# Kernel tuning notes

Measured on AMD Instinct MI355X. Metric: run time of the kernel, lower is better.

Reference implementation:

```python
import jax, jax.numpy as jnp
import numpy as np

N = 20000      # num_sr == num_tg entities
D = 256        # ent_dim
DR = 256       # rel_dim
RNUM = 1000    # number of relations
Q = 128        # SVD rank
H = 4          # n_head
L = 2          # layers
E_RAND = 640000  # random edges (avg degree 32); N self-loops appended
LEAK = 0.2
EPS_LN = 1e-5


def _l2norm(x):
    # F.normalize(x, dim=1, p=2)
    return x / jnp.maximum(jnp.linalg.norm(x, axis=1, keepdims=True), 1e-12)


def _gat(x, src, dst, W, a_s, a_d):
    """Multi-head GAT layer on an edge list; heads are averaged so out dim == in dim.
    x: [N,D], W: [H,D,D], a_s/a_d: [H,D]."""
    n = x.shape[0]
    h = jnp.einsum('nd,hde->nhe', x, W)                  # [N,H,D]
    es = jnp.einsum('nhe,he->nh', h, a_s)                # [N,H]
    ed = jnp.einsum('nhe,he->nh', h, a_d)                # [N,H]
    e = jax.nn.leaky_relu(es[src] + ed[dst], LEAK)       # [E,H]
    # segment softmax over incoming edges of each dst node
    m = jax.ops.segment_max(e, dst, num_segments=n)      # [N,H]
    ex = jnp.exp(e - m[dst])
    den = jax.ops.segment_sum(ex, dst, num_segments=n)   # [N,H]
    attn = ex / (den[dst] + 1e-16)                       # [E,H]
    out = jax.ops.segment_sum(attn[:, :, None] * h[src], dst, num_segments=n)  # [N,H,D]
    return jax.nn.elu(out).mean(axis=1)                  # head average -> [N,D]


def _mha(x, wq, bq, wk, bk, wv, bv, fc_w, fc_b, ln_g, ln_b):
    """Standard post-norm multi-head self-attention over the 'ranges' axis. x: [N,R,D]."""
    n, r, d = x.shape
    def split(y):  # [N,R,H*D] -> [N,H,R,D]
        return y.reshape(n, r, H, d).transpose(0, 2, 1, 3)
    q, k, v = split(x @ wq + bq), split(x @ wk + bk), split(x @ wv + bv)
    attn = jax.nn.softmax(jnp.einsum('nhqd,nhkd->nhqk', q, k) / jnp.sqrt(jnp.float32(d)), axis=-1)
    o = jnp.einsum('nhqk,nhkd->nhqd', attn, v).transpose(0, 2, 1, 3).reshape(n, r, H * d)
    o = o @ fc_w + fc_b + x                              # output proj + residual
    mu = o.mean(-1, keepdims=True)
    var = o.var(-1, keepdims=True)
    return (o - mu) / jnp.sqrt(var + EPS_LN) * ln_g + ln_b


def _rel_agg(adj_in, adj_out, rel):
    # sparse-dense mm + row-sum normalize + concat (direct=True branch)
    ri = (adj_in @ rel) / (adj_in.sum(-1, keepdims=True) + 1e-5)
    ro = (adj_out @ rel) / (adj_out.sum(-1, keepdims=True) + 1e-5)
    return jnp.concatenate([ri, ro], axis=-1)            # [N, 2*DR]


def _forward(ent_sr, ent_tg, rel_sr, rel_tg, alpha,
             u_mul_s_sr, vt_sr, u_mul_s_tg, vt_tg,
             rel_adj_sr_in, rel_adj_sr_out, rel_adj_tg_in, rel_adj_tg_out,
             gat_W, gat_a_src, gat_a_dst,
             wq, bq, wk, bk, wv, bv, fc_w, fc_b, ln_g, ln_b,
             edges_sr, edges_tg):
    # --- Relation Aggregator (direct=True, phase='eval': aug == aggregated) ---
    sr_rel = _rel_agg(rel_adj_sr_in, rel_adj_sr_out, rel_sr)
    tg_rel = _rel_agg(rel_adj_tg_in, rel_adj_tg_out, rel_tg)
    aug_sr_rel, aug_tg_rel = sr_rel, tg_rel

    # --- Global Structure Aggregator: SVD-based propagation ---
    e_sr, e_tg = ent_sr, ent_tg
    for _ in range(L):
        g_sr = u_mul_s_sr @ (vt_sr @ e_sr)               # [N,Q]@([Q,N]@[N,D])
        g_tg = u_mul_s_tg @ (vt_tg @ e_tg)
        e_sr = jax.nn.relu(alpha * g_sr + (1.0 - alpha) * e_sr)
        e_tg = jax.nn.relu(alpha * g_tg + (1.0 - alpha) * e_tg)
    aug_sr = e_sr + ent_sr
    aug_tg = e_tg + ent_tg

    # --- Attentive Neighbor Aggregator (res=True; eval => dropout = identity) ---
    x_sr, x_tg = ent_sr, ent_tg
    sr_list, tg_list = [x_sr], [x_tg]
    for l in range(L):
        x_sr = _l2norm(_gat(x_sr, edges_sr[0], edges_sr[1], gat_W[l], gat_a_src[l], gat_a_dst[l]))
        x_tg = _l2norm(_gat(x_tg, edges_tg[0], edges_tg[1], gat_W[l], gat_a_src[l], gat_a_dst[l]))
        sr_list.append(x_sr)
        tg_list.append(x_tg)

    # --- multi-range neighborhood fusion ---
    sr = _mha(jnp.stack(sr_list, axis=1), wq, bq, wk, bk, wv, bv, fc_w, fc_b, ln_g, ln_b).mean(axis=1)
    tg = _mha(jnp.stack(tg_list, axis=1), wq, bq, wk, bk, wv, bv, fc_w, fc_b, ln_g, ln_b).mean(axis=1)

    # --- final fusion: neighbors + relation semantics ---
    sr_out = jnp.concatenate([sr, sr_rel], axis=-1)
    tg_out = jnp.concatenate([tg, tg_rel], axis=-1)
    aug_sr_out = jnp.concatenate([aug_sr, aug_sr_rel], axis=-1)
    aug_tg_out = jnp.concatenate([aug_tg, aug_tg_rel], axis=-1)
    return (sr_out, tg_out, aug_sr_out, aug_tg_out)


def setup_inputs() -> dict:
    key = jax.random.key(0)
    ks = jax.random.split(key, 32)
    def nrm(k, shape, s):
        return jax.random.normal(k, shape, jnp.float32) * s
    def edges(k):
        e = jax.random.randint(k, (2, E_RAND), 0, N, dtype=jnp.int32)
        loops = jnp.arange(N, dtype=jnp.int32)
        return jnp.concatenate([e, jnp.stack([loops, loops])], axis=1)  # [2, E_RAND+N]
    inp = {
        'ent_sr': nrm(ks[0], (N, D), 0.1),
        'ent_tg': nrm(ks[1], (N, D), 0.1),
        'rel_sr': nrm(ks[2], (RNUM, DR), 0.1),
        'rel_tg': nrm(ks[3], (RNUM, DR), 0.1),
        'alpha': jnp.float32(0.5),
        'u_mul_s_sr': nrm(ks[4], (N, Q), 0.05),
        'vt_sr': nrm(ks[5], (Q, N), 0.05),
        'u_mul_s_tg': nrm(ks[6], (N, Q), 0.05),
        'vt_tg': nrm(ks[7], (Q, N), 0.05),
        'rel_adj_sr_in': jax.random.uniform(ks[8], (N, RNUM), jnp.float32),
        'rel_adj_sr_out': jax.random.uniform(ks[9], (N, RNUM), jnp.float32),
        'rel_adj_tg_in': jax.random.uniform(ks[10], (N, RNUM), jnp.float32),
        'rel_adj_tg_out': jax.random.uniform(ks[11], (N, RNUM), jnp.float32),
        'gat_W': nrm(ks[12], (L, H, D, D), 1.0 / np.sqrt(D)),
        'gat_a_src': nrm(ks[13], (L, H, D), 1.0 / np.sqrt(D)),
        'gat_a_dst': nrm(ks[14], (L, H, D), 1.0 / np.sqrt(D)),
        'wq': nrm(ks[15], (D, H * D), 1.0 / np.sqrt(D)),
        'bq': jnp.zeros((H * D,), jnp.float32),
        'wk': nrm(ks[16], (D, H * D), 1.0 / np.sqrt(D)),
        'bk': jnp.zeros((H * D,), jnp.float32),
        'wv': nrm(ks[17], (D, H * D), 1.0 / np.sqrt(D)),
        'bv': jnp.zeros((H * D,), jnp.float32),
        'fc_w': nrm(ks[18], (H * D, D), 1.0 / np.sqrt(H * D)),
        'fc_b': jnp.zeros((D,), jnp.float32),
        'ln_g': jnp.ones((D,), jnp.float32),
        'ln_b': jnp.zeros((D,), jnp.float32),
        'edges_sr': edges(ks[19]),
        'edges_tg': edges(ks[20]),
    }
    return inp


def reference(ent_sr, ent_tg, rel_sr, rel_tg, alpha,
              u_mul_s_sr, vt_sr, u_mul_s_tg, vt_tg,
              rel_adj_sr_in, rel_adj_sr_out, rel_adj_tg_in, rel_adj_tg_out,
              gat_W, gat_a_src, gat_a_dst,
              wq, bq, wk, bk, wv, bv, fc_w, fc_b, ln_g, ln_b,
              edges_sr, edges_tg):
    return _forward(ent_sr, ent_tg, rel_sr, rel_tg, alpha,
                    u_mul_s_sr, vt_sr, u_mul_s_tg, vt_tg,
                    rel_adj_sr_in, rel_adj_sr_out, rel_adj_tg_in, rel_adj_tg_out,
                    gat_W, gat_a_src, gat_a_dst,
                    wq, bq, wk, bk, wv, bv, fc_w, fc_b, ln_g, ln_b,
                    edges_sr, edges_tg)
```

## Files before the change

### kernel.cpp

```cpp
#include <hip/hip_runtime.h>
#include <stdint.h>

typedef unsigned short u16;
typedef __bf16 bf16x8 __attribute__((ext_vector_type(8)));
typedef float f32x4 __attribute__((ext_vector_type(4)));

#define DEV static __device__ __forceinline__

DEV float bf2f(u16 u) { unsigned v = ((unsigned)u) << 16; float f; __builtin_memcpy(&f, &v, 4); return f; }
DEV u16 f2bf(float f) {
  unsigned x; __builtin_memcpy(&x, &f, 4);
  x += 0x7FFFu + ((x >> 16) & 1u);
  return (u16)(x >> 16);
}
DEV float wred_sum(float v) { for (int m = 32; m; m >>= 1) v += __shfl_xor(v, m); return v; }
DEV float wred_max(float v) { for (int m = 32; m; m >>= 1) v = fmaxf(v, __shfl_xor(v, m)); return v; }
DEV void wred_max4(f32x4& v) {
  for (int m = 32; m; m >>= 1) {
#pragma unroll
    for (int i = 0; i < 4; ++i) v[i] = fmaxf(v[i], __shfl_xor(v[i], m));
  }
}
DEV void wred_sum4(f32x4& v) {
  for (int m = 32; m; m >>= 1) {
#pragma unroll
    for (int i = 0; i < 4; ++i) v[i] += __shfl_xor(v[i], m);
  }
}

enum { M_ATOMIC = 0, M_SCALE2, M_BLEND, M_BF16, M_BF16B, M_F32B };

template <int MODE>
__global__ __launch_bounds__(256) void k_gemm(
    const u16* __restrict__ A, const u16* __restrict__ B,
    int M, int lda, int ldb, int Ksteps, int kper,
    void* __restrict__ C1v, float* __restrict__ C2, int ldc,
    const float* __restrict__ rowsum, const float* __restrict__ ein, int ldein,
    const float* __restrict__ alphap, const float* __restrict__ bias,
    long hA, long hB, long hC)
{
  __shared__ u16 As[4096], Bs[4096];
  const int tid = threadIdx.x, lane = tid & 63, wid = tid >> 6;
  const long m0 = (long)blockIdx.x * 128, n0 = (long)blockIdx.y * 128;
  int ks, kend;
  long chead = 0;
  if (hA | hB | hC) {
    A += (long)blockIdx.z * hA;
    B += (long)blockIdx.z * hB;
    chead = (long)blockIdx.z * hC;
    ks = 0; kend = Ksteps;
  } else {
    ks = blockIdx.z * kper;
    kend = ks + kper; if (kend > Ksteps) kend = Ksteps;
  }

  const u16 *ag[2], *bg[2];
  u16 *al[2], *bl[2];
#pragma unroll
  for (int i = 0; i < 2; ++i) {
    int s = (wid * 2 + i) * 64 + lane;
    int row = s >> 2, cs = (s & 3) ^ ((row >> 1) & 3);
    ag[i] = A + (m0 + row) * (long)lda + cs * 8;
    bg[i] = B + (n0 + row) * (long)ldb + cs * 8;
    al[i] = As + (wid * 2 + i) * 512;
    bl[i] = Bs + (wid * 2 + i) * 512;
  }
  const int kq = lane >> 4, rr = lane & 15;
  const int wm = wid >> 1, wn = wid & 1;

// ... 23 lines not shown
      for (int j = 0; j < 4; ++j)
        acc[i][j] = __builtin_amdgcn_mfma_f32_16x16x32_bf16(af[i], bff[j], acc[i][j], 0, 0, 0);
    __syncthreads();
  }

  float* Cf = (float*)C1v;
  u16* Cu = (u16*)C1v;
  const int r4 = (lane >> 4) << 2;
#pragma unroll
  for (int i = 0; i < 4; ++i) {
#pragma unroll
    for (int rg = 0; rg < 4; ++rg) {
      long row = m0 + wm * 64 + i * 16 + r4 + rg;
      if (row >= M) continue;
      float scale = 0.f, al_ = 0.f, ml_ = 0.f;
      if (MODE == M_SCALE2) scale = 1.f / (rowsum[row] + 1e-5f);
      if (MODE == M_BLEND) { al_ = *alphap; ml_ = 1.f - al_; }
#pragma unroll
      for (int j = 0; j < 4; ++j) {
        long col = n0 + wn * 64 + j * 16 + rr;
        float v = acc[i][j][rg];
        long idx = chead + row * (long)ldc + col;
        if (MODE == M_ATOMIC) atomicAdd(Cf + idx, v);
        else if (MODE == M_SCALE2) { float sv = v * scale; Cf[idx] = sv; C2[idx] = sv; }
        else if (MODE == M_BLEND) { float e = ein[row * (long)ldein + col]; Cf[idx] = fmaxf(al_ * v + ml_ * e, 0.f); }
        else if (MODE == M_BF16) Cu[idx] = f2bf(v);
        else if (MODE == M_BF16B) Cu[idx] = f2bf(v + bias[col]);
        else if (MODE == M_F32B) Cf[idx] = v + bias[col];
      }
    }
  }
}

__global__ void k_cvt(const float* __restrict__ in, u16* __restrict__ out, long R, long C, long Cp, long ostride)
{
  long idx = (long)blockIdx.x * blockDim.x + threadIdx.x;
  long cw = Cp >> 3;
  if (idx >= R * cw) return;
// ... 34 lines not shown
    tile[tr + i * 16][tc4 + 3] = v[3];
  }
  __syncthreads();
  int wc = t >> 4, wr4 = (t & 15) << 2;
#pragma unroll
  for (int i = 0; i < 4; ++i) {
    int c = wc + i * 16;
    u16 o[4];
#pragma unroll
    for (int k2 = 0; k2 < 4; ++k2) o[k2] = f2bf(tile[wr4 + k2][c]);
    unsigned long long pk; __builtin_memcpy(&pk, o, 8);
    *(unsigned long long*)(out + ((long)b * C + (ct << 6) + c) * Rp + (rt << 6) + wr4) = pk;
  }
}

__global__ __launch_bounds__(256) void k_adj(const float* __restrict__ in, u16* __restrict__ out,
                                             float* __restrict__ rowsum, int C, int Cp)
{
  int r = blockIdx.x, t = threadIdx.x;
  f32x4 v = {0.f, 0.f, 0.f, 0.f};
  int c = t << 2;
  if (c + 3 < C) v = *(const f32x4*)(in + (long)r * C + c);
  u16 o[4];
#pragma unroll
  for (int i = 0; i < 4; ++i) o[i] = f2bf(v[i]);
  unsigned long long pk; __builtin_memcpy(&pk, o, 8);
  *(unsigned long long*)(out + (long)r * Cp + c) = pk;
  float s = wred_sum(v[0] + v[1] + v[2] + v[3]);
  __shared__ float ws4[4];
  if ((t & 63) == 0) ws4[t >> 6] = s;
  __syncthreads();
  if (t == 0) rowsum[r] = ws4[0] + ws4[1] + ws4[2] + ws4[3];
}

__global__ void k_zero_i(int* p, int n) { for (int i = blockIdx.x * blockDim.x + threadIdx.x; i < n; i += gridDim.x * blockDim.x) p[i] = 0; }
__global__ void k_zero_f(float* p, int n) { for (int i = blockIdx.x * blockDim.x + threadIdx.x; i < n; i += gridDim.x * blockDim.x) p[i] = 0.f; }
__global__ void k_copy_i(const int* __restrict__ a, int* __restrict__ b, int n) { for (int i = blockIdx.x * blockDim.x + threadIdx.x; i < n; i += gridDim.x * blockDim.x) b[i] = a[i]; }
__global__ void k_hist(const int* __restrict__ dst, int* __restrict__ deg, int E)
{ for (int i = blockIdx.x * blockDim.x + threadIdx.x; i < E; i += gridDim.x * blockDim.x) atomicAdd(&deg[dst[i]], 1); }
__global__ void k_scatter(const int* __restrict__ src, const int* __restrict__ dst, int* __restrict__ cur,
                          int* __restrict__ srcs, int E)
{
  for (int i = blockIdx.x * blockDim.x + threadIdx.x; i < E; i += gridDim.x * blockDim.x) {
    int p = atomicAdd(&cur[dst[i]], 1);
    srcs[p] = src[i];
  }
}
__global__ void k_scan(const int* __restrict__ deg, int* __restrict__ off, int n)
{
  __shared__ int buf[1024];
  __shared__ int carry;
  int t = threadIdx.x;
  if (t == 0) { carry = 0; off[0] = 0; }
  __syncthreads();
  for (int base = 0; base < n; base += 1024) {
    int v = (base + t < n) ? deg[base + t] : 0;
    buf[t] = v;
    __syncthreads();
    for (int s = 1; s < 1024; s <<= 1) {
      int x = (t >= s) ? buf[t - s] : 0;
      __syncthreads();
      buf[t] += x;
      __syncthreads();
    }
    if (base + t < n) off[base + t + 1] = buf[t] + carry;
    int tot = buf[1023];
    __syncthreads();
    if (t == 0) carry += tot;
    __syncthreads();
  }
}

__global__ __launch_bounds__(256) void k_esed(const u16* __restrict__ h, const float* __restrict__ as_,
                                              const float* __restrict__ ad_, float* __restrict__ esq,
                                              float* __restrict__ ed, signed char* __restrict__ q8, int N)
{
  int n = blockIdx.x, t = threadIdx.x, hd = t >> 6, l = t & 63;
  long base = (long)n * 1024 + hd * 256 + (l << 2);
  ushort4 hv = *(const ushort4*)(h + base);
  float h0 = bf2f(hv.x), h1 = bf2f(hv.y), h2 = bf2f(hv.z), h3 = bf2f(hv.w);
  const float* ap = as_ + hd * 256 + (l << 2);
  const float* dp = ad_ + hd * 256 + (l << 2);
  float ps = h0 * ap[0] + h1 * ap[1] + h2 * ap[2] + h3 * ap[3];
  float pd = h0 * dp[0] + h1 * dp[1] + h2 * dp[2] + h3 * dp[3];
  ps = wred_sum(ps); pd = wred_sum(pd);
// ... 4 lines not shown
  qb[0] = (signed char)__float2int_rn(h0 * rsc);
  qb[1] = (signed char)__float2int_rn(h1 * rsc);
  qb[2] = (signed char)__float2int_rn(h2 * rsc);
  qb[3] = (signed char)__float2int_rn(h3 * rsc);
  int qw; __builtin_memcpy(&qw, qb, 4);
  *(int*)(q8 + base) = qw;
  if (l == 0) {
    esq[n * 8 + hd] = ps;
    esq[n * 8 + 4 + hd] = amax * (1.f / 127.f);
    ed[n * 4 + hd] = pd;
  }
}

__global__ __launch_bounds__(256) void k_gat(const signed char* __restrict__ q8,
                                             const float* __restrict__ esq, const float* __restrict__ ed,
                                             const int* __restrict__ off, const int* __restrict__ srcs,
                                             u16* __restrict__ xout, int N)
{
  int t = threadIdx.x, w = t >> 6, l = t & 63;
  int n = blockIdx.x * 4 + w;
  if (n >= N) return;
  int e0 = off[n], deg = off[n + 1] - e0;
  f32x4 edv = *(const f32x4*)(ed + (long)n * 4);

  f32x4 m = {-1e30f, -1e30f, -1e30f, -1e30f};
  f32x4 psum = {0.f, 0.f, 0.f, 0.f};
  f32x4 acc0 = {0.f, 0.f, 0.f, 0.f};
  f32x4 acc1 = {0.f, 0.f, 0.f, 0.f};
  f32x4 acc2 = {0.f, 0.f, 0.f, 0.f};
  f32x4 acc3 = {0.f, 0.f, 0.f, 0.f};
  const long loff = l << 2;

  for (int base = 0; base < deg; base += 64) {
    int cnt = min(64, deg - base);
    bool act = l < cnt;
    int s = 0;
    f32x4 v = {-1e30f, -1e30f, -1e30f, -1e30f};
    if (act) {
// ... 80 lines not shown
  for (int j = 0; j < 256; ++j) {
    a1 += wk[(long)d * 1024 + h * 256 + j] * bq[h * 256 + j];
    a2 += wq[(long)d * 1024 + h * 256 + j] * bk[h * 256 + j];
    a3 += bv[h * 256 + j] * fcw[(long)(h * 256 + j) * 256 + d];
  }
  vq1[t] = a1; vq2[t] = a2; beff2[t] = a3;
  if (d == 0) {
    float s = 0.f;
    for (int j = 0; j < 256; ++j) s += bq[h * 256 + j] * bk[h * 256 + j];
    s3[h] = s;
  }
}

__global__ __launch_bounds__(256) void k_score2(const u16* __restrict__ x, const u16* __restrict__ kg,
                                                const float* __restrict__ vq1, const float* __restrict__ vq2,
                                                const float* __restrict__ s3, float* __restrict__ attn, int N)
{
  int n = blockIdx.x, t = threadIdx.x, hd = t >> 6, l = t & 63;
  int i4 = l << 2;
  f32x4 xr[3], kc[3];
#pragma unroll
  for (int r = 0; r < 3; ++r) {
    ushort4 a = *(const ushort4*)(x + ((long)n * 3 + r) * 256 + i4);
    xr[r][0] = bf2f(a.x); xr[r][1] = bf2f(a.y); xr[r][2] = bf2f(a.z); xr[r][3] = bf2f(a.w);
    ushort4 b = *(const ushort4*)(kg + ((long)n * 3 + r) * 1024 + hd * 256 + i4);
    kc[r][0] = bf2f(b.x); kc[r][1] = bf2f(b.y); kc[r][2] = bf2f(b.z); kc[r][3] = bf2f(b.w);
  }
  f32x4 v1 = *(const f32x4*)(vq1 + hd * 256 + i4);
  f32x4 v2 = *(const f32x4*)(vq2 + hd * 256 + i4);
  float red[15];
#pragma unroll
  for (int r = 0; r < 3; ++r)
#pragma unroll
    for (int c = 0; c < 3; ++c) {
      f32x4 p = xr[r] * kc[c];
      red[r * 3 + c] = p[0] + p[1] + p[2] + p[3];
    }
#pragma unroll
  for (int c = 0; c < 3; ++c) {
    f32x4 p1 = xr[c] * v1;
    f32x4 p2 = xr[c] * v2;
    red[9 + c] = p1[0] + p1[1] + p1[2] + p1[3];
    red[12 + c] = p2[0] + p2[1] + p2[2] + p2[3];
  }
#pragma unroll
  for (int i = 0; i < 15; ++i) red[i] = wred_sum(red[i]);
  if (l == 0) {
    float s3h = s3[hd];
    float* out = attn + (long)n * 36 + hd * 9;
#pragma unroll
    for (int r = 0; r < 3; ++r) {
      float v0 = (red[r * 3 + 0] + red[9 + 0] + red[12 + r] + s3h) * 0.0625f;
      float v1_ = (red[r * 3 + 1] + red[9 + 1] + red[12 + r] + s3h) * 0.0625f;
      float v2_ = (red[r * 3 + 2] + red[9 + 2] + red[12 + r] + s3h) * 0.0625f;
      float mm = fmaxf(v0, fmaxf(v1_, v2_));
      float e0 = __expf(v0 - mm), e1 = __expf(v1_ - mm), e2 = __expf(v2_ - mm);
      float rs = 1.f / (e0 + e1 + e2);
      out[r * 3 + 0] = e0 * rs; out[r * 3 + 1] = e1 * rs; out[r * 3 + 2] = e2 * rs;
    }
  }
}

__global__ __launch_bounds__(256) void k_cln(const u16* __restrict__ vf, const float* __restrict__ attn,
                                             const u16* __restrict__ x, const float* __restrict__ fcb,
                                             const float* __restrict__ g, const float* __restrict__ b,
                                             float* __restrict__ out, int N)
{
  int n = blockIdx.x, t = threadIdx.x, w = t >> 6, l = t & 63;
  __shared__ float aa[36];
  __shared__ float ybuf[3][256];
  if (t < 36) aa[t] = attn[(long)n * 36 + t];
  __syncthreads();
  if (w < 3) {
    int d4 = l << 2;
    f32x4 acc = {0.f, 0.f, 0.f, 0.f};
#pragma unroll
    for (int h = 0; h < 4; ++h)
#pragma unroll
      for (int rp = 0; rp < 3; ++rp) {
        float wgt = aa[h * 9 + w * 3 + rp];
        ushort4 vv = *(const ushort4*)(vf + ((long)n * 3 + rp) * 1024 + h * 256 + d4);
        acc[0] += wgt * bf2f(vv.x); acc[1] += wgt * bf2f(vv.y);
        acc[2] += wgt * bf2f(vv.z); acc[3] += wgt * bf2f(vv.w);
      }
    f32x4 fb = *(const f32x4*)(fcb + d4);
    ushort4 xu = *(const ushort4*)(x + ((long)n * 3 + w) * 256 + d4);
    acc[0] += fb[0] + bf2f(xu.x); acc[1] += fb[1] + bf2f(xu.y);
    acc[2] += fb[2] + bf2f(xu.z); acc[3] += fb[3] + bf2f(xu.w);
    float s1 = acc[0] + acc[1] + acc[2] + acc[3];
    float s2 = acc[0] * acc[0] + acc[1] * acc[1] + acc[2] * acc[2] + acc[3] * acc[3];
    s1 = wred_sum(s1); s2 = wred_sum(s2);
    float mu = s1 * 0.00390625f;
    float var = s2 * 0.00390625f - mu * mu;
    float rs = rsqrtf(var + 1e-5f);
#pragma unroll
    for (int i = 0; i < 4; ++i) {
      int d = d4 + i;
      ybuf[w][d] = (acc[i] - mu) * rs * g[d] + b[d];
    }
  }
  __syncthreads();
  if (t < 64) {
#pragma unroll
    for (int i = 0; i < 4; ++i) {
      int d = (t << 2) + i;
      out[(long)n * 768 + d] = (ybuf[0][d] + ybuf[1][d] + ybuf[2][d]) * (1.f / 3.f);
    }
  }
}

__global__ void k_aug(const float* __restrict__ e, const float* __restrict__ ent, float* __restrict__ out, int N)
{
  long i = (long)blockIdx.x * blockDim.x + threadIdx.x;
  if (i >= (long)N * 64) return;
  long n = i >> 6; int d4 = (int)(i & 63) << 2;
  f32x4 a = *(const f32x4*)(e + n * 256 + d4);
  f32x4 c = *(const f32x4*)(ent + n * 256 + d4);
  *(f32x4*)(out + n * 768 + d4) = a + c;
}

extern "C" void kernel_launch(void* const* d_in, const int* in_sizes, int n_in,
                              void* d_out, int out_size, void* d_ws, size_t ws_size,
                              hipStream_t stream)
{
  (void)n_in; (void)out_size; (void)ws_size;
  const int N = 20000, NP = 20096, RNUM = 1000, RP = 1024;
  const int NT2 = NP + N;
  const int Es = in_sizes[26] / 2, Et = in_sizes[27] / 2;

  const float* ent_sr = (const float*)d_in[0];
  const float* ent_tg = (const float*)d_in[1];
  const float* rel_in[2] = {(const float*)d_in[2], (const float*)d_in[3]};
  const float* alphap = (const float*)d_in[4];
  const float* ums[2] = {(const float*)d_in[5], (const float*)d_in[7]};
  const float* vt[2]  = {(const float*)d_in[6], (const float*)d_in[8]};
  const float* adj[4] = {(const float*)d_in[9], (const float*)d_in[10], (const float*)d_in[11], (const float*)d_in[12]};
  const float* gat_W  = (const float*)d_in[13];
  const float* gat_as = (const float*)d_in[14];
  const float* gat_ad = (const float*)d_in[15];
  const float* wq = (const float*)d_in[16]; const float* bq = (const float*)d_in[17];
  const float* wk = (const float*)d_in[18]; const float* bk = (const float*)d_in[19];
  const float* wv = (const float*)d_in[20]; const float* bv = (const float*)d_in[21];
  const float* fcw = (const float*)d_in[22]; const float* fcb = (const float*)d_in[23];
  const float* lng = (const float*)d_in[24]; const float* lnb = (const float*)d_in[25];
  const int* edges[2] = {(const int*)d_in[26], (const int*)d_in[27]};
  const int Ecnt[2] = {Es, Et};

  float* out0 = (float*)d_out;
  float* out1 = out0 + (size_t)N * 768;
  float* out2 = out1 + (size_t)N * 768;
  float* out3 = out2 + (size_t)N * 768;

  char* wsp = (char*)d_ws; size_t wo = 0;
  auto alloc = [&](size_t bytes) { void* p = wsp + wo; wo = (wo + bytes + 255) & ~(size_t)255; return p; };

  u16* A_sr = (u16*)alloc((size_t)NP * 768 * 2);
  u16* A_tg = (u16*)alloc((size_t)NP * 768 * 2);
  u16* QBUF = (u16*)alloc((size_t)60160 * 1024 * 2);
  u16* KBUF = (u16*)alloc((size_t)60160 * 1024 * 2);
  float* OFIN = (float*)alloc((size_t)60160 * 256 * 4);
  float* rowsum = (float*)alloc((size_t)N * 4);
  u16* relT[2] = {(u16*)alloc(256 * RP * 2), (u16*)alloc(256 * RP * 2)};
  u16* WtG = (u16*)alloc((size_t)2 * 1024 * 256 * 2);
  u16* fcT = (u16*)alloc(256 * 1024 * 2);
  u16* wqB = (u16*)alloc(256 * 1024 * 2);
  u16* wkB = (u16*)alloc(256 * 1024 * 2);
  u16* wvB = (u16*)alloc(256 * 1024 * 2);
  u16* gT  = (u16*)alloc((size_t)4 * 256 * 256 * 2);
  u16* vfT = (u16*)alloc((size_t)4 * 256 * 256 * 2);
  float* vq1 = (float*)alloc(1024 * 4);
  float* vq2 = (float*)alloc(1024 * 4);
  float* beff2 = (float*)alloc(1024 * 4);
  float* s3b = (float*)alloc(4 * 4);
  float* esqb = (float*)alloc((size_t)NT2 * 8 * 4);
  float* edb = (float*)alloc((size_t)NT2 * 4 * 4);
  float* attn = (float*)alloc((size_t)N * 36 * 4);
  int* off_[2]; int* cur_[2]; int* srcs_[2];
  for (int s = 0; s < 2; ++s) {
    off_[s] = (int*)alloc((size_t)(N + 4) * 4);
    cur_[s] = (int*)alloc((size_t)(N + 4) * 4);
    srcs_[s] = (int*)alloc((size_t)Ecnt[s] * 4);
  }
  float* tT = (float*)alloc(256 * 128 * 4);
  u16* tTb = (u16*)alloc(256 * 128 * 2);

  u16* hbuf = QBUF;
  u16* adjb = (u16*)OFIN;
  float* e_b[2];
  e_b[0] = (float*)KBUF;
  e_b[1] = e_b[0] + (size_t)N * 256;
  u16* eT = (u16*)(e_b[1] + (size_t)N * 256);
  u16* vtb[2]; u16* umb[2];
  vtb[0] = eT + (size_t)256 * NP;
  vtb[1] = vtb[0] + (size_t)128 * NP;
  umb[0] = vtb[1] + (size_t)128 * NP;
  umb[1] = umb[0] + (size_t)NP * 128;
  signed char* q8buf = (signed char*)KBUF;
  u16* kgbuf = KBUF;

  u16* A_s[2] = {A_sr, A_tg};
  const float* ent_s[2] = {ent_sr, ent_tg};
  float* outm[2] = {out0, out1};
  float* outa[2] = {out2, out3};

  auto cvt = [&](const float* in, u16* out, long R, long C, long Cp, long ostr) {
    long total = R * (Cp >> 3);
    int blocks = (int)((total + 255) / 256);
    k_cvt<<<blocks, 256, 0, stream>>>(in, out, R, C, Cp, ostr);
  };
  auto cvtT = [&](const float* in, u16* out, int Bh, int R, int C, int Rp) {
    int blocks = (Rp >> 6) * (C >> 6) * Bh;
    k_cvtT<<<blocks, 256, 0, stream>>>(in, out, Bh, R, C, Rp);
  };
  auto gemm = [&](int mode, const u16* A, const u16* B, int M, int lda, int ldb, int Kp, int Nt, int splits,
                  void* C1, float* C2, int ldc, const float* rs, const float* ein, int ldein,
                  const float* alp, const float* bias, long hA = 0, long hB = 0, long hC = 0) {
    int Ks = Kp >> 5;
    int kper = (splits > 1 && !hC) ? (Ks + splits - 1) / splits : Ks;
    dim3 g((M + 127) >> 7, Nt, splits);
    switch (mode) {
      case M_ATOMIC: k_gemm<M_ATOMIC><<<g, 256, 0, stream>>>(A, B, M, lda, ldb, Ks, kper, C1, C2, ldc, rs, ein, ldein, alp, bias, hA, hB, hC); break;
      case M_SCALE2: k_gemm<M_SCALE2><<<g, 256, 0, stream>>>(A, B, M, lda, ldb, Ks, kper, C1, C2, ldc, rs, ein, ldein, alp, bias, hA, hB, hC); break;
      case M_BLEND:  k_gemm<M_BLEND><<<g, 256, 0, stream>>>(A, B, M, lda, ldb, Ks, kper, C1, C2, ldc, rs, ein, ldein, alp, bias, hA, hB, hC); break;
      case M_BF16:   k_gemm<M_BF16><<<g, 256, 0, stream>>>(A, B, M, lda, ldb, Ks, kper, C1, C2, ldc, rs, ein, ldein, alp, bias, hA, hB, hC); break;
      case M_BF16B:  k_gemm<M_BF16B><<<g, 256, 0, stream>>>(A, B, M, lda, ldb, Ks, kper, C1, C2, ldc, rs, ein, ldein, alp, bias, hA, hB, hC); break;
      case M_F32B:   k_gemm<M_F32B><<<g, 256, 0, stream>>>(A, B, M, lda, ldb, Ks, kper, C1, C2, ldc, rs, ein, ldein, alp, bias, hA, hB, hC); break;
    }
  };

  for (int s = 0; s < 2; ++s) {
    k_zero_i<<<80, 256, 0, stream>>>(cur_[s], N);
    k_hist<<<1024, 256, 0, stream>>>(edges[s] + Ecnt[s], cur_[s], Ecnt[s]);
    k_scan<<<1, 1024, 0, stream>>>(cur_[s], off_[s], N);
    k_copy_i<<<80, 256, 0, stream>>>(off_[s], cur_[s], N);
    k_scatter<<<1024, 256, 0, stream>>>(edges[s], edges[s] + Ecnt[s], cur_[s], srcs_[s], Ecnt[s]);
  }

  cvtT(rel_in[0], relT[0], 1, RNUM, 256, RP);
  cvtT(rel_in[1], relT[1], 1, RNUM, 256, RP);
  struct RelOp { const float* a; u16* rt; float* c1; float* c2; } relops[4] = {
      {adj[0], relT[0], out0 + 256, out2 + 256},
      {adj[1], relT[0], out0 + 512, out2 + 512},
      {adj[2], relT[1], out1 + 256, out3 + 256},
      {adj[3], relT[1], out1 + 512, out3 + 512},
  };
  for (int i = 0; i < 4; ++i) {
    k_adj<<<N, 256, 0, stream>>>(relops[i].a, adjb, rowsum, RNUM, RP);
    gemm(M_SCALE2, adjb, relops[i].rt, N, RP, RP, RP, 2, 1,
         relops[i].c1, relops[i].c2, 768, rowsum, nullptr, 0, nullptr, nullptr);
  }

  cvt(vt[0], vtb[0], 128, N, NP, NP);
  cvt(vt[1], vtb[1], 128, N, NP, NP);
  cvt(ums[0], umb[0], N, 128, 128, 128);
  cvt(ums[1], umb[1], N, 128, 128, 128);
  for (int s = 0; s < 2; ++s) {
    for (int l = 0; l < 2; ++l) {
      const float* esrc = l ? (const float*)e_b[s] : ent_s[s];
      cvtT(esrc, eT, 1, N, 256, NP);
      k_zero_f<<<128, 256, 0, stream>>>(tT, 256 * 128);
      gemm(M_ATOMIC, eT, vtb[s], 256, NP, NP, NP, 1, 128, tT, nullptr, 128,
           nullptr, nullptr, 0, nullptr, nullptr);
      cvt(tT, tTb, 256, 128, 128, 128);
      gemm(M_BLEND, umb[s], tTb, N, 128, 128, 128, 2, 1, e_b[s], nullptr, 256,
           nullptr, esrc, 256, alphap, nullptr);
    }
    k_aug<<<(N * 64 + 255) / 256, 256, 0, stream>>>(e_b[s], ent_s[s], outa[s], N);
  }

  cvt(ent_sr, A_sr, N, 256, 256, 768);
  cvt(ent_tg, A_tg, N, 256, 256, 768);
  cvtT(gat_W, WtG, 4, 256, 256, 256);
  cvtT(gat_W + 4 * 256 * 256, WtG + (size_t)1024 * 256, 4, 256, 256, 256);
  for (int l = 0; l < 2; ++l) {
    gemm(M_BF16, A_sr + l * 256, WtG + (size_t)l * 1024 * 256, NT2, 768, 256, 256, 8, 1,
         hbuf, nullptr, 1024, nullptr, nullptr, 0, nullptr, nullptr);
    k_esed<<<NT2, 256, 0, stream>>>(hbuf, gat_as + l * 1024, gat_ad + l * 1024, esqb, edb, q8buf, NT2);
    for (int s = 0; s < 2; ++s) {
      size_t ofs = s ? (size_t)NP : 0;
      k_gat<<<(N + 3) / 4, 256, 0, stream>>>(q8buf + ofs * 1024, esqb + ofs * 8, edb + ofs * 4,
                                             off_[s], srcs_[s], A_s[s] + (l + 1) * 256, N);
    }
  }

  cvt(wq, wqB, 256, 1024, 1024, 1024);
  cvt(wk, wkB, 256, 1024, 1024, 1024);
  cvt(wv, wvB, 256, 1024, 1024, 1024);
  cvtT(fcw, fcT, 1, 1024, 256, 1024);
  k_bias2<<<4, 256, 0, stream>>>(wq, wk, fcw, bq, bk, bv, vq1, vq2, beff2, s3b);
  gemm(M_BF16, wqB, wkB, 256, 1024, 1024, 256, 2, 4, gT, nullptr, 256,
       nullptr, nullptr, 0, nullptr, nullptr, 256, 256, 65536);
  gemm(M_BF16, fcT, wvB, 256, 1024, 1024, 256, 2, 4, vfT, nullptr, 256,
       nullptr, nullptr, 0, nullptr, nullptr, 256, 256, 65536);

  for (int s = 0; s < 2; ++s) {
    gemm(M_BF16, A_s[s], gT, 3 * N, 256, 256, 256, 8, 1, kgbuf, nullptr, 1024,
         nullptr, nullptr, 0, nullptr, nullptr);
    k_score2<<<N, 256, 0, stream>>>(A_s[s], kgbuf, vq1, vq2, s3b, attn, N);
    gemm(M_BF16B, A_s[s], vfT, 3 * N, 256, 256, 256, 8, 1, QBUF, nullptr, 1024,
         nullptr, nullptr, 0, nullptr, beff2);
    k_cln<<<N, 256, 0, stream>>>(QBUF, attn, A_s[s], fcb, lng, lnb, outm[s], N);
  }
}
```

Measured before the change: 1.926 ms.

## Batch sr/tg pipelines into merged launches and replace atomic split-K with partial reduction

Merges the separate source and target passes into single launches: k_adj4 over four adjacency matrices, batched GEMMs through a head/split z index, k_gat, k_score2, k_cln and k_aug each handle both sides via blockIdx.y. The atomic split-K GEMM for the SVD projection becomes a partial-sum GEMM (M_PART) followed by a k_red reduction kernel, which removes the zero-fill and the atomics. The prefix scan now gives each thread a serial chunk before one block scan, cutting the number of barrier rounds. This lowers launch count and the cost of small serial kernels, but uses more workspace and adds a reduction pass.

After: 1.732 ms. 1.11x faster.

```diff
diff --git a/kernel.cpp b/kernel.cpp
--- a/kernel.cpp
+++ b/kernel.cpp
@@ -28,7 +28,7 @@
   }
 }
 
-enum { M_ATOMIC = 0, M_SCALE2, M_BLEND, M_BF16, M_BF16B, M_F32B };
+enum { M_ATOMIC = 0, M_SCALE2, M_BLEND, M_BF16, M_BF16B, M_F32B, M_PART };
 
 template <int MODE>
 __global__ __launch_bounds__(256) void k_gemm(
@@ -37,22 +37,28 @@
     void* __restrict__ C1v, float* __restrict__ C2, int ldc,
     const float* __restrict__ rowsum, const float* __restrict__ ein, int ldein,
     const float* __restrict__ alphap, const float* __restrict__ bias,
-    long hA, long hB, long hC)
+    long hA, long hB, long hC, int nsplit, long hE)
 {
   __shared__ u16 As[4096], Bs[4096];
   const int tid = threadIdx.x, lane = tid & 63, wid = tid >> 6;
   const long m0 = (long)blockIdx.x * 128, n0 = (long)blockIdx.y * 128;
   int ks, kend;
   long chead = 0;
+  int hz = 0;
   if (hA | hB | hC) {
-    A += (long)blockIdx.z * hA;
-    B += (long)blockIdx.z * hB;
-    chead = (long)blockIdx.z * hC;
-    ks = 0; kend = Ksteps;
+    int z = blockIdx.z;
+    hz = z / nsplit;
+    int sp = z - hz * nsplit;
+    A += (long)hz * hA;
+    B += (long)hz * hB;
+    chead = (MODE == M_PART) ? (long)z * hC : (long)hz * hC;
+    ks = sp * kper;
+    kend = ks + kper; if (kend > Ksteps) kend = Ksteps;
   } else {
     ks = blockIdx.z * kper;
     kend = ks + kper; if (kend > Ksteps) kend = Ksteps;
   }
+  if (MODE == M_BLEND) ein += (long)hz * hE;
 
   const u16 *ag[2], *bg[2];
   u16 *al[2], *bl[2];
@@ -106,7 +112,7 @@
       long row = m0 + wm * 64 + i * 16 + r4 + rg;
       if (row >= M) continue;
       float scale = 0.f, al_ = 0.f, ml_ = 0.f;
-      if (MODE == M_SCALE2) scale = 1.f / (rowsum[row] + 1e-5f);
+      if (MODE == M_SCALE2) scale = 1.f / (rowsum[(long)hz * M + row] + 1e-5f);
       if (MODE == M_BLEND) { al_ = *alphap; ml_ = 1.f - al_; }
 #pragma unroll
       for (int j = 0; j < 4; ++j) {
@@ -114,6 +120,7 @@
         float v = acc[i][j][rg];
         long idx = chead + row * (long)ldc + col;
         if (MODE == M_ATOMIC) atomicAdd(Cf + idx, v);
+        else if (MODE == M_PART) Cf[idx] = v;
         else if (MODE == M_SCALE2) { float sv = v * scale; Cf[idx] = sv; C2[idx] = sv; }
         else if (MODE == M_BLEND) { float e = ein[row * (long)ldein + col]; Cf[idx] = fmaxf(al_ * v + ml_ * e, 0.f); }
         else if (MODE == M_BF16) Cu[idx] = f2bf(v);
@@ -178,10 +185,14 @@
   }
 }
 
-__global__ __launch_bounds__(256) void k_adj(const float* __restrict__ in, u16* __restrict__ out,
-                                             float* __restrict__ rowsum, int C, int Cp)
-{
-  int r = blockIdx.x, t = threadIdx.x;
+__global__ __launch_bounds__(256) void k_adj4(const float* __restrict__ a0, const float* __restrict__ a1,
+                                              const float* __restrict__ a2, const float* __restrict__ a3,
+                                              u16* __restrict__ o01, u16* __restrict__ o23,
+                                              float* __restrict__ rowsum, int C, int Cp, int N)
+{
+  int r = blockIdx.x, pl = blockIdx.y, t = threadIdx.x;
+  const float* in = pl == 0 ? a0 : pl == 1 ? a1 : pl == 2 ? a2 : a3;
+  u16* out = pl < 2 ? o01 + (size_t)pl * N * Cp : o23 + (size_t)(pl - 2) * N * Cp;
   f32x4 v = {0.f, 0.f, 0.f, 0.f};
   int c = t << 2;
   if (c + 3 < C) v = *(const f32x4*)(in + (long)r * C + c);
@@ -194,11 +205,20 @@
   __shared__ float ws4[4];
   if ((t & 63) == 0) ws4[t >> 6] = s;
   __syncthreads();
-  if (t == 0) rowsum[r] = ws4[0] + ws4[1] + ws4[2] + ws4[3];
+  if (t == 0) rowsum[(long)pl * N + r] = ws4[0] + ws4[1] + ws4[2] + ws4[3];
+}
+
+__global__ void k_red(const float* __restrict__ P, float* __restrict__ o, int NS)
+{
+  int i = blockIdx.x * 256 + threadIdx.x;
+  int h = i >> 15, rem = i & 32767;
+  const float* p = P + (long)h * NS * 32768 + rem;
+  float s = 0.f;
+  for (int k = 0; k < NS; ++k) s += p[(long)k * 32768];
+  o[i] = s;
 }
 
 __global__ void k_zero_i(int* p, int n) { for (int i = blockIdx.x * blockDim.x + threadIdx.x; i < n; i += gridDim.x * blockDim.x) p[i] = 0; }
-__global__ void k_zero_f(float* p, int n) { for (int i = blockIdx.x * blockDim.x + threadIdx.x; i < n; i += gridDim.x * blockDim.x) p[i] = 0.f; }
 __global__ void k_copy_i(const int* __restrict__ a, int* __restrict__ b, int n) { for (int i = blockIdx.x * blockDim.x + threadIdx.x; i < n; i += gridDim.x * blockDim.x) b[i] = a[i]; }
 __global__ void k_hist(const int* __restrict__ dst, int* __restrict__ deg, int E)
 { for (int i = blockIdx.x * blockDim.x + threadIdx.x; i < E; i += gridDim.x * blockDim.x) atomicAdd(&deg[dst[i]], 1); }
@@ -210,29 +230,25 @@
     srcs[p] = src[i];
   }
 }
-__global__ void k_scan(const int* __restrict__ deg, int* __restrict__ off, int n)
-{
-  __shared__ int buf[1024];
-  __shared__ int carry;
+__global__ __launch_bounds__(1024) void k_scan(const int* __restrict__ deg, int* __restrict__ off, int n)
+{
+  __shared__ int bsum[1024];
   int t = threadIdx.x;
-  if (t == 0) { carry = 0; off[0] = 0; }
+  int per = (n + 1023) >> 10;
+  int s0 = t * per, s1 = s0 + per; if (s1 > n) s1 = n;
+  int s = 0;
+  for (int i = s0; i < s1; ++i) s += deg[i];
+  bsum[t] = s;
   __syncthreads();
-  for (int base = 0; base < n; base += 1024) {
-    int v = (base + t < n) ? deg[base + t] : 0;
-    buf[t] = v;
+  for (int d = 1; d < 1024; d <<= 1) {
+    int x = (t >= d) ? bsum[t - d] : 0;
     __syncthreads();
-    for (int s = 1; s < 1024; s <<= 1) {
-      int x = (t >= s) ? buf[t - s] : 0;
-      __syncthreads();
-      buf[t] += x;
-      __syncthreads();
-    }
-    if (base + t < n) off[base + t + 1] = buf[t] + carry;
-    int tot = buf[1023];
+    bsum[t] += x;
     __syncthreads();
-    if (t == 0) carry += tot;
-    __syncthreads();
-  }
+  }
+  if (t == 0) off[0] = 0;
+  int run = t ? bsum[t - 1] : 0;
+  for (int i = s0; i < s1; ++i) { run += deg[i]; off[i + 1] = run; }
 }
 
 __global__ __launch_bounds__(256) void k_esed(const u16* __restrict__ h, const float* __restrict__ as_,
@@ -267,14 +283,22 @@
 
 __global__ __launch_bounds__(256) void k_gat(const signed char* __restrict__ q8,
                                              const float* __restrict__ esq, const float* __restrict__ ed,
-                                             const int* __restrict__ off, const int* __restrict__ srcs,
-                                             u16* __restrict__ xout, int N)
+                                             const int* __restrict__ off0, const int* __restrict__ srcs0,
+                                             const int* __restrict__ off1, const int* __restrict__ srcs1,
+                                             u16* __restrict__ x0, u16* __restrict__ x1, int N, int NPq)
 {
   int t = threadIdx.x, w = t >> 6, l = t & 63;
   int n = blockIdx.x * 4 + w;
   if (n >= N) return;
+  int side = blockIdx.y;
+  const int* off = side ? off1 : off0;
+  const int* srcs = side ? srcs1 : srcs0;
+  u16* xout = side ? x1 : x0;
+  size_t ofs = side ? (size_t)NPq : 0;
+  q8 += ofs * 1024; esq += ofs * 8;
+
   int e0 = off[n], deg = off[n + 1] - e0;
-  f32x4 edv = *(const f32x4*)(ed + (long)n * 4);
+  f32x4 edv = *(const f32x4*)(ed + (ofs + n) * 4);
 
   f32x4 m = {-1e30f, -1e30f, -1e30f, -1e30f};
   f32x4 psum = {0.f, 0.f, 0.f, 0.f};
@@ -385,16 +409,18 @@
 
 __global__ __launch_bounds__(256) void k_score2(const u16* __restrict__ x, const u16* __restrict__ kg,
                                                 const float* __restrict__ vq1, const float* __restrict__ vq2,
-                                                const float* __restrict__ s3, float* __restrict__ attn, int N)
-{
-  int n = blockIdx.x, t = threadIdx.x, hd = t >> 6, l = t & 63;
+                                                const float* __restrict__ s3, float* __restrict__ attn,
+                                                int N, int NPq)
+{
+  int n = blockIdx.x, side = blockIdx.y, t = threadIdx.x, hd = t >> 6, l = t & 63;
+  long rbase = (long)side * 3 * NPq + (long)n * 3;
   int i4 = l << 2;
   f32x4 xr[3], kc[3];
 #pragma unroll
   for (int r = 0; r < 3; ++r) {
-    ushort4 a = *(const ushort4*)(x + ((long)n * 3 + r) * 256 + i4);
+    ushort4 a = *(const ushort4*)(x + (rbase + r) * 256 + i4);
     xr[r][0] = bf2f(a.x); xr[r][1] = bf2f(a.y); xr[r][2] = bf2f(a.z); xr[r][3] = bf2f(a.w);
-    ushort4 b = *(const ushort4*)(kg + ((long)n * 3 + r) * 1024 + hd * 256 + i4);
+    ushort4 b = *(const ushort4*)(kg + (rbase + r) * 1024 + hd * 256 + i4);
     kc[r][0] = bf2f(b.x); kc[r][1] = bf2f(b.y); kc[r][2] = bf2f(b.z); kc[r][3] = bf2f(b.w);
   }
   f32x4 v1 = *(const f32x4*)(vq1 + hd * 256 + i4);
@@ -418,7 +444,7 @@
   for (int i = 0; i < 15; ++i) red[i] = wred_sum(red[i]);
   if (l == 0) {
     float s3h = s3[hd];
-    float* out = attn + (long)n * 36 + hd * 9;
+    float* out = attn + ((long)side * N + n) * 36 + hd * 9;
 #pragma unroll
     for (int r = 0; r < 3; ++r) {
       float v0 = (red[r * 3 + 0] + red[9 + 0] + red[12 + r] + s3h) * 0.0625f;
@@ -435,12 +461,15 @@
 __global__ __launch_bounds__(256) void k_cln(const u16* __restrict__ vf, const float* __restrict__ attn,
                                              const u16* __restrict__ x, const float* __restrict__ fcb,
                                              const float* __restrict__ g, const float* __restrict__ b,
-                                             float* __restrict__ out, int N)
-{
-  int n = blockIdx.x, t = threadIdx.x, w = t >> 6, l = t & 63;
+                                             float* __restrict__ out0, float* __restrict__ out1,
+                                             int N, int NPq)
+{
+  int n = blockIdx.x, side = blockIdx.y, t = threadIdx.x, w = t >> 6, l = t & 63;
+  long rbase = (long)side * 3 * NPq + (long)n * 3;
+  float* out = (side ? out1 : out0) + (long)n * 768;
   __shared__ float aa[36];
   __shared__ float ybuf[3][256];
-  if (t < 36) aa[t] = attn[(long)n * 36 + t];
+  if (t < 36) aa[t] = attn[((long)side * N + n) * 36 + t];
   __syncthreads();
   if (w < 3) {
     int d4 = l << 2;
@@ -450,12 +479,12 @@
 #pragma unroll
       for (int rp = 0; rp < 3; ++rp) {
         float wgt = aa[h * 9 + w * 3 + rp];
-        ushort4 vv = *(const ushort4*)(vf + ((long)n * 3 + rp) * 1024 + h * 256 + d4);
+        ushort4 vv = *(const ushort4*)(vf + (rbase + rp) * 1024 + h * 256 + d4);
         acc[0] += wgt * bf2f(vv.x); acc[1] += wgt * bf2f(vv.y);
         acc[2] += wgt * bf2f(vv.z); acc[3] += wgt * bf2f(vv.w);
       }
     f32x4 fb = *(const f32x4*)(fcb + d4);
-    ushort4 xu = *(const ushort4*)(x + ((long)n * 3 + w) * 256 + d4);
+    ushort4 xu = *(const ushort4*)(x + (rbase + w) * 256 + d4);
     acc[0] += fb[0] + bf2f(xu.x); acc[1] += fb[1] + bf2f(xu.y);
     acc[2] += fb[2] + bf2f(xu.z); acc[3] += fb[3] + bf2f(xu.w);
     float s1 = acc[0] + acc[1] + acc[2] + acc[3];
@@ -475,19 +504,23 @@
 #pragma unroll
     for (int i = 0; i < 4; ++i) {
       int d = (t << 2) + i;
-      out[(long)n * 768 + d] = (ybuf[0][d] + ybuf[1][d] + ybuf[2][d]) * (1.f / 3.f);
-    }
-  }
-}
-
-__global__ void k_aug(const float* __restrict__ e, const float* __restrict__ ent, float* __restrict__ out, int N)
+      out[d] = (ybuf[0][d] + ybuf[1][d] + ybuf[2][d]) * (1.f / 3.f);
+    }
+  }
+}
+
+__global__ void k_aug(const float* __restrict__ e, const float* __restrict__ ent0,
+                      const float* __restrict__ ent1, float* __restrict__ out, int N)
 {
   long i = (long)blockIdx.x * blockDim.x + threadIdx.x;
-  if (i >= (long)N * 64) return;
-  long n = i >> 6; int d4 = (int)(i & 63) << 2;
-  f32x4 a = *(const f32x4*)(e + n * 256 + d4);
+  if (i >= (long)N * 128) return;
+  int side = i >= (long)N * 64;
+  long ii = side ? i - (long)N * 64 : i;
+  const float* ent = side ? ent1 : ent0;
+  long n = ii >> 6; int d4 = (int)(ii & 63) << 2;
+  f32x4 a = *(const f32x4*)(e + ((long)side * N + n) * 256 + d4);
   f32x4 c = *(const f32x4*)(ent + n * 256 + d4);
-  *(f32x4*)(out + n * 768 + d4) = a + c;
+  *(f32x4*)(out + ((long)side * N + n) * 768 + d4) = a + c;
 }
 
 extern "C" void kernel_launch(void* const* d_in, const int* in_sizes, int n_in,
@@ -497,6 +530,7 @@
   (void)n_in; (void)out_size; (void)ws_size;
   const int N = 20000, NP = 20096, RNUM = 1000, RP = 1024;
   const int NT2 = NP + N;
+  const int NS = 64;
   const int Es = in_sizes[26] / 2, Et = in_sizes[27] / 2;
 
   const float* ent_sr = (const float*)d_in[0];
@@ -527,10 +561,10 @@
 
   u16* A_sr = (u16*)alloc((size_t)NP * 768 * 2);
   u16* A_tg = (u16*)alloc((size_t)NP * 768 * 2);
-  u16* QBUF = (u16*)alloc((size_t)60160 * 1024 * 2);
-  u16* KBUF = (u16*)alloc((size_t)60160 * 1024 * 2);
-  float* OFIN = (float*)alloc((size_t)60160 * 256 * 4);
-  float* rowsum = (float*)alloc((size_t)N * 4);
+  u16* QBUF = (u16*)alloc((size_t)3 * NT2 * 1024 * 2);
+  u16* KBUF = (u16*)alloc((size_t)3 * NT2 * 1024 * 2);
+  float* PART = (float*)alloc((size_t)2 * NS * 32768 * 4);
+  float* rowsum = (float*)alloc((size_t)4 * N * 4);
   u16* relT[2] = {(u16*)alloc(256 * RP * 2), (u16*)alloc(256 * RP * 2)};
   u16* WtG = (u16*)alloc((size_t)2 * 1024 * 256 * 2);
   u16* fcT = (u16*)alloc(256 * 1024 * 2);
@@ -545,34 +579,28 @@
   float* s3b = (float*)alloc(4 * 4);
   float* esqb = (float*)alloc((size_t)NT2 * 8 * 4);
   float* edb = (float*)alloc((size_t)NT2 * 4 * 4);
-  float* attn = (float*)alloc((size_t)N * 36 * 4);
+  float* attn = (float*)alloc((size_t)2 * N * 36 * 4);
   int* off_[2]; int* cur_[2]; int* srcs_[2];
   for (int s = 0; s < 2; ++s) {
     off_[s] = (int*)alloc((size_t)(N + 4) * 4);
     cur_[s] = (int*)alloc((size_t)(N + 4) * 4);
     srcs_[s] = (int*)alloc((size_t)Ecnt[s] * 4);
   }
-  float* tT = (float*)alloc(256 * 128 * 4);
-  u16* tTb = (u16*)alloc(256 * 128 * 2);
+  float* tT2 = (float*)alloc((size_t)2 * 256 * 128 * 4);
+  u16* tTb2 = (u16*)alloc((size_t)2 * 256 * 128 * 2);
 
   u16* hbuf = QBUF;
-  u16* adjb = (u16*)OFIN;
-  float* e_b[2];
-  e_b[0] = (float*)KBUF;
-  e_b[1] = e_b[0] + (size_t)N * 256;
-  u16* eT = (u16*)(e_b[1] + (size_t)N * 256);
-  u16* vtb[2]; u16* umb[2];
-  vtb[0] = eT + (size_t)256 * NP;
-  vtb[1] = vtb[0] + (size_t)128 * NP;
-  umb[0] = vtb[1] + (size_t)128 * NP;
-  umb[1] = umb[0] + (size_t)NP * 128;
+  u16* vfbuf = QBUF;
+  u16* adjbQ = QBUF;
+  u16* adjbK = KBUF;
+  float* e_b = (float*)KBUF;
+  u16* eT = (u16*)(e_b + (size_t)2 * N * 256);
+  u16* vtb0 = eT + (size_t)2 * 256 * NP;
+  u16* umb0 = vtb0 + (size_t)2 * 128 * NP;
   signed char* q8buf = (signed char*)KBUF;
   u16* kgbuf = KBUF;
 
-  u16* A_s[2] = {A_sr, A_tg};
   const float* ent_s[2] = {ent_sr, ent_tg};
-  float* outm[2] = {out0, out1};
-  float* outa[2] = {out2, out3};
 
   auto cvt = [&](const float* in, u16* out, long R, long C, long Cp, long ostr) {
     long total = R * (Cp >> 3);
@@ -583,19 +611,24 @@
     int blocks = (Rp >> 6) * (C >> 6) * Bh;
     k_cvtT<<<blocks, 256, 0, stream>>>(in, out, Bh, R, C, Rp);
   };
-  auto gemm = [&](int mode, const u16* A, const u16* B, int M, int lda, int ldb, int Kp, int Nt, int splits,
+  auto gemm = [&](int mode, const u16* A, const u16* B, int M, int lda, int ldb, int Kp, int Nt,
+                  int zdim, int nsplit,
                   void* C1, float* C2, int ldc, const float* rs, const float* ein, int ldein,
-                  const float* alp, const float* bias, long hA = 0, long hB = 0, long hC = 0) {
+                  const float* alp, const float* bias,
+                  long hA = 0, long hB = 0, long hC = 0, long hE = 0) {
     int Ks = Kp >> 5;
-    int kper = (splits > 1 && !hC) ? (Ks + splits - 1) / splits : Ks;
-    dim3 g((M + 127) >> 7, Nt, splits);
+    bool hmode = (hA | hB | hC) != 0;
+    int kper = hmode ? (Ks + nsplit - 1) / nsplit
+                     : (zdim > 1 ? (Ks + zdim - 1) / zdim : Ks);
+    dim3 g((M + 127) >> 7, Nt, zdim);
     switch (mode) {
-      case M_ATOMIC: k_gemm<M_ATOMIC><<<g, 256, 0, stream>>>(A, B, M, lda, ldb, Ks, kper, C1, C2, ldc, rs, ein, ldein, alp, bias, hA, hB, hC); break;
-      case M_SCALE2: k_gemm<M_SCALE2><<<g, 256, 0, stream>>>(A, B, M, lda, ldb, Ks, kper, C1, C2, ldc, rs, ein, ldein, alp, bias, hA, hB, hC); break;
-      case M_BLEND:  k_gemm<M_BLEND><<<g, 256, 0, stream>>>(A, B, M, lda, ldb, Ks, kper, C1, C2, ldc, rs, ein, ldein, alp, bias, hA, hB, hC); break;
-      case M_BF16:   k_gemm<M_BF16><<<g, 256, 0, stream>>>(A, B, M, lda, ldb, Ks, kper, C1, C2, ldc, rs, ein, ldein, alp, bias, hA, hB, hC); break;
-      case M_BF16B:  k_gemm<M_BF16B><<<g, 256, 0, stream>>>(A, B, M, lda, ldb, Ks, kper, C1, C2, ldc, rs, ein, ldein, alp, bias, hA, hB, hC); break;
-      case M_F32B:   k_gemm<M_F32B><<<g, 256, 0, stream>>>(A, B, M, lda, ldb, Ks, kper, C1, C2, ldc, rs, ein, ldein, alp, bias, hA, hB, hC); break;
+      case M_ATOMIC: k_gemm<M_ATOMIC><<<g, 256, 0, stream>>>(A, B, M, lda, ldb, Ks, kper, C1, C2, ldc, rs, ein, ldein, alp, bias, hA, hB, hC, nsplit, hE); break;
+      case M_SCALE2: k_gemm<M_SCALE2><<<g, 256, 0, stream>>>(A, B, M, lda, ldb, Ks, kper, C1, C2, ldc, rs, ein, ldein, alp, bias, hA, hB, hC, nsplit, hE); break;
+      case M_BLEND:  k_gemm<M_BLEND><<<g, 256, 0, stream>>>(A, B, M, lda, ldb, Ks, kper, C1, C2, ldc, rs, ein, ldein, alp, bias, hA, hB, hC, nsplit, hE); break;
+      case M_BF16:   k_gemm<M_BF16><<<g, 256, 0, stream>>>(A, B, M, lda, ldb, Ks, kper, C1, C2, ldc, rs, ein, ldein, alp, bias, hA, hB, hC, nsplit, hE); break;
+      case M_BF16B:  k_gemm<M_BF16B><<<g, 256, 0, stream>>>(A, B, M, lda, ldb, Ks, kper, C1, C2, ldc, rs, ein, ldein, alp, bias, hA, hB, hC, nsplit, hE); break;
+      case M_F32B:   k_gemm<M_F32B><<<g, 256, 0, stream>>>(A, B, M, lda, ldb, Ks, kper, C1, C2, ldc, rs, ein, ldein, alp, bias, hA, hB, hC, nsplit, hE); break;
+      case M_PART:   k_gemm<M_PART><<<g, 256, 0, stream>>>(A, B, M, lda, ldb, Ks, kper, C1, C2, ldc, rs, ein, ldein, alp, bias, hA, hB, hC, nsplit, hE); break;
     }
   };
 
@@ -609,49 +642,55 @@
 
   cvtT(rel_in[0], relT[0], 1, RNUM, 256, RP);
   cvtT(rel_in[1], relT[1], 1, RNUM, 256, RP);
-  struct RelOp { const float* a; u16* rt; float* c1; float* c2; } relops[4] = {
-      {adj[0], relT[0], out0 + 256, out2 + 256},
-      {adj[1], relT[0], out0 + 512, out2 + 512},
-      {adj[2], relT[1], out1 + 256, out3 + 256},
-      {adj[3], relT[1], out1 + 512, out3 + 512},
-  };
-  for (int i = 0; i < 4; ++i) {
-    k_adj<<<N, 256, 0, stream>>>(relops[i].a, adjb, rowsum, RNUM, RP);
-    gemm(M_SCALE2, adjb, relops[i].rt, N, RP, RP, RP, 2, 1,
-         relops[i].c1, relops[i].c2, 768, rowsum, nullptr, 0, nullptr, nullptr);
-  }
-
-  cvt(vt[0], vtb[0], 128, N, NP, NP);
-  cvt(vt[1], vtb[1], 128, N, NP, NP);
-  cvt(ums[0], umb[0], N, 128, 128, 128);
-  cvt(ums[1], umb[1], N, 128, 128, 128);
-  for (int s = 0; s < 2; ++s) {
-    for (int l = 0; l < 2; ++l) {
-      const float* esrc = l ? (const float*)e_b[s] : ent_s[s];
-      cvtT(esrc, eT, 1, N, 256, NP);
-      k_zero_f<<<128, 256, 0, stream>>>(tT, 256 * 128);
-      gemm(M_ATOMIC, eT, vtb[s], 256, NP, NP, NP, 1, 128, tT, nullptr, 128,
-           nullptr, nullptr, 0, nullptr, nullptr);
-      cvt(tT, tTb, 256, 128, 128, 128);
-      gemm(M_BLEND, umb[s], tTb, N, 128, 128, 128, 2, 1, e_b[s], nullptr, 256,
-           nullptr, esrc, 256, alphap, nullptr);
-    }
-    k_aug<<<(N * 64 + 255) / 256, 256, 0, stream>>>(e_b[s], ent_s[s], outa[s], N);
-  }
+  {
+    dim3 ga(N, 4);
+    k_adj4<<<ga, 256, 0, stream>>>(adj[0], adj[1], adj[2], adj[3], adjbQ, adjbK, rowsum, RNUM, RP, N);
+  }
+  gemm(M_SCALE2, adjbQ, relT[0], N, RP, RP, RP, 2, 2, 1,
+       out0 + 256, out2 + 256, 768, rowsum, nullptr, 0, nullptr, nullptr,
+       (long)N * RP, 0, 256);
+  gemm(M_SCALE2, adjbK, relT[1], N, RP, RP, RP, 2, 2, 1,
+       out1 + 256, out3 + 256, 768, rowsum + 2 * N, nullptr, 0, nullptr, nullptr,
+       (long)N * RP, 0, 256);
+
+  cvt(vt[0], vtb0, 128, N, NP, NP);
+  cvt(vt[1], vtb0 + (size_t)128 * NP, 128, N, NP, NP);
+  cvt(ums[0], umb0, N, 128, 128, 128);
+  cvt(ums[1], umb0 + (size_t)NP * 128, N, 128, 128, 128);
+  for (int l = 0; l < 2; ++l) {
+    if (l == 0) {
+      cvtT(ent_sr, eT, 1, N, 256, NP);
+      cvtT(ent_tg, eT + (size_t)256 * NP, 1, N, 256, NP);
+    } else {
+      cvtT(e_b, eT, 2, N, 256, NP);
+    }
+    gemm(M_PART, eT, vtb0, 256, NP, NP, NP, 1, 2 * NS, NS,
+         PART, nullptr, 128, nullptr, nullptr, 0, nullptr, nullptr,
+         (long)256 * NP, (long)128 * NP, 32768);
+    k_red<<<256, 256, 0, stream>>>(PART, tT2, NS);
+    cvt(tT2, tTb2, 512, 128, 128, 128);
+    if (l == 0) {
+      for (int s = 0; s < 2; ++s)
+        gemm(M_BLEND, umb0 + (size_t)s * NP * 128, tTb2 + (size_t)s * 32768, N, 128, 128, 128, 2, 1, 1,
+             e_b + (size_t)s * N * 256, nullptr, 256, nullptr, ent_s[s], 256, alphap, nullptr);
+    } else {
+      gemm(M_BLEND, umb0, tTb2, N, 128, 128, 128, 2, 2, 1,
+           e_b, nullptr, 256, nullptr, e_b, 256, alphap, nullptr,
+           (long)NP * 128, 32768, (long)N * 256, (long)N * 256);
+    }
+  }
+  k_aug<<<(int)(((long)N * 128 + 255) / 256), 256, 0, stream>>>(e_b, ent_sr, ent_tg, out2, N);
 
   cvt(ent_sr, A_sr, N, 256, 256, 768);
   cvt(ent_tg, A_tg, N, 256, 256, 768);
-  cvtT(gat_W, WtG, 4, 256, 256, 256);
-  cvtT(gat_W + 4 * 256 * 256, WtG + (size_t)1024 * 256, 4, 256, 256, 256);
+  cvtT(gat_W, WtG, 8, 256, 256, 256);
   for (int l = 0; l < 2; ++l) {
-    gemm(M_BF16, A_sr + l * 256, WtG + (size_t)l * 1024 * 256, NT2, 768, 256, 256, 8, 1,
+    gemm(M_BF16, A_sr + l * 256, WtG + (size_t)l * 1024 * 256, NT2, 768, 256, 256, 8, 1, 1,
          hbuf, nullptr, 1024, nullptr, nullptr, 0, nullptr, nullptr);
     k_esed<<<NT2, 256, 0, stream>>>(hbuf, gat_as + l * 1024, gat_ad + l * 1024, esqb, edb, q8buf, NT2);
-    for (int s = 0; s < 2; ++s) {
-      size_t ofs = s ? (size_t)NP : 0;
-      k_gat<<<(N + 3) / 4, 256, 0, stream>>>(q8buf + ofs * 1024, esqb + ofs * 8, edb + ofs * 4,
-                                             off_[s], srcs_[s], A_s[s] + (l + 1) * 256, N);
-    }
+    dim3 gg((N + 3) / 4, 2);
+    k_gat<<<gg, 256, 0, stream>>>(q8buf, esqb, edb, off_[0], srcs_[0], off_[1], srcs_[1],
+                                  A_sr + (l + 1) * 256, A_tg + (l + 1) * 256, N, NP);
   }
 
   cvt(wq, wqB, 256, 1024, 1024, 1024);
@@ -659,17 +698,21 @@
   cvt(wv, wvB, 256, 1024, 1024, 1024);
   cvtT(fcw, fcT, 1, 1024, 256, 1024);
   k_bias2<<<4, 256, 0, stream>>>(wq, wk, fcw, bq, bk, bv, vq1, vq2, beff2, s3b);
-  gemm(M_BF16, wqB, wkB, 256, 1024, 1024, 256, 2, 4, gT, nullptr, 256,
+  gemm(M_BF16, wqB, wkB, 256, 1024, 1024, 256, 2, 4, 1, gT, nullptr, 256,
        nullptr, nullptr, 0, nullptr, nullptr, 256, 256, 65536);
-  gemm(M_BF16, fcT, wvB, 256, 1024, 1024, 256, 2, 4, vfT, nullptr, 256,
+  gemm(M_BF16, fcT, wvB, 256, 1024, 1024, 256, 2, 4, 1, vfT, nullptr, 256,
        nullptr, nullptr, 0, nullptr, nullptr, 256, 256, 65536);
 
-  for (int s = 0; s < 2; ++s) {
-    gemm(M_BF16, A_s[s], gT, 3 * N, 256, 256, 256, 8, 1, kgbuf, nullptr, 1024,
-         nullptr, nullptr, 0, nullptr, nullptr);
-    k_score2<<<N, 256, 0, stream>>>(A_s[s], kgbuf, vq1, vq2, s3b, attn, N);
-    gemm(M_BF16B, A_s[s], vfT, 3 * N, 256, 256, 256, 8, 1, QBUF, nullptr, 1024,
-         nullptr, nullptr, 0, nullptr, beff2);
-    k_cln<<<N, 256, 0, stream>>>(QBUF, attn, A_s[s], fcb, lng, lnb, outm[s], N);
-  }
-}
+  gemm(M_BF16, A_sr, gT, 3 * NT2, 256, 256, 256, 8, 1, 1, kgbuf, nullptr, 1024,
+       nullptr, nullptr, 0, nullptr, nullptr);
+  {
+    dim3 gs(N, 2);
+    k_score2<<<gs, 256, 0, stream>>>(A_sr, kgbuf, vq1, vq2, s3b, attn, N, NP);
+  }
+  gemm(M_BF16B, A_sr, vfT, 3 * NT2, 256, 256, 256, 8, 1, 1, vfbuf, nullptr, 1024,
+       nullptr, nullptr, 0, nullptr, beff2);
+  {
+    dim3 gc(N, 2);
+    k_cln<<<gc, 256, 0, stream>>>(vfbuf, attn, A_sr, fcb, lng, lnb, out0, out1, N, NP);
+  }
+}
```
